# Performance work log

Hardware: AMD Instinct MI355X
Metric: run time of the kernel (lower is better)

## Reference

```python
import jax, jax.numpy as jnp
import numpy as np

N_NODES = 10000
N_EDGES = 100000
IN_FEATS = 64
OUT_FEATS = 64
N_EDGE_TYPES = 10


def setup_inputs() -> dict:
    key = jax.random.key(0)
    k_feat, k_src, k_dst, k_ord, k_emb = jax.random.split(key, 5)
    feat = jax.random.normal(k_feat, (N_NODES, IN_FEATS), dtype=jnp.float32)
    src = jax.random.randint(k_src, (N_EDGES,), 0, N_NODES, dtype=jnp.int32)
    dst = jax.random.randint(k_dst, (N_EDGES,), 0, N_NODES, dtype=jnp.int32)
    order = jax.random.randint(k_ord, (N_EDGES,), 0, N_EDGE_TYPES, dtype=jnp.int32)
    # xavier-uniform-like init for the relation-weight embedding table
    emb_weight = jax.random.normal(k_emb, (N_EDGE_TYPES, IN_FEATS * OUT_FEATS), dtype=jnp.float32) * 0.02
    bias = jnp.zeros((OUT_FEATS,), dtype=jnp.float32)
    return {"feat": feat, "src": src, "dst": dst, "order": order,
            "emb_weight": emb_weight, "bias": bias}


def reference(feat, src, dst, order, emb_weight, bias):
    n_nodes, in_feats = feat.shape
    out_feats = emb_weight.shape[1] // in_feats
    n_edges = src.shape[0]
    ones_e = jnp.ones((n_edges,), dtype=feat.dtype)

    # norm='both': scale source features by out_degree^{-1/2}
    out_deg = jnp.clip(jax.ops.segment_sum(ones_e, src, num_segments=n_nodes), 1.0)
    feat_n = feat * (out_deg ** -0.5)[:, None]

    # per-edge relation weight gather: [E, out, in]
    w = emb_weight[order].reshape(n_edges, out_feats, in_feats)
    h_src = feat_n[src]                              # [E, in]
    msg = jnp.einsum('eoi,ei->eo', w, h_src)         # [E, out]

    # scatter-sum aggregate to destination nodes
    rst = jax.ops.segment_sum(msg, dst, num_segments=n_nodes)  # [N, out]

    # post-norm by in_degree^{-1/2}
    in_deg = jnp.clip(jax.ops.segment_sum(ones_e, dst, num_segments=n_nodes), 1.0)
    rst = rst * (in_deg ** -0.5)[:, None]
    return rst + bias
```

## Files before the change

kernel.cpp:

```cpp
#include <hip/hip_runtime.h>
#include <stdint.h>


typedef __attribute__((ext_vector_type(8))) short short8;
typedef __attribute__((ext_vector_type(4))) float f32x4;

constexpr int N_NODES = 10000;
constexpr int N_EDGES = 100000;
constexpr int F = 64;
constexpr int R = 10;
constexpr int BLOCK = 256;
constexpr int EPG = 32;
constexpr int CAP = 16384;
constexpr int GPR = CAP / EPG;
constexpr int N_GROUPS = R * GPR;
constexpr int CAPN = 64;

union U8 { uint32_t u[4]; short8 s; };

__device__ inline uint32_t pk_hi(float x, float y) {
    uint32_t bx = __float_as_uint(x), by = __float_as_uint(y);
    return (bx >> 16) | (by & 0xFFFF0000u);
}
__device__ inline uint32_t pk_lo(float x, float y) {
    uint32_t bx = __float_as_uint(x), by = __float_as_uint(y);
    float lx = x - __uint_as_float(bx & 0xFFFF0000u);
    float ly = y - __uint_as_float(by & 0xFFFF0000u);
    return (__float_as_uint(lx) >> 16) | (__float_as_uint(ly) & 0xFFFF0000u);
}

__global__ void k_count(const int* __restrict__ src, const int* __restrict__ dst,
                        const int* __restrict__ order, const float* __restrict__ emb,
                        int* deg_out, int* deg_in, int* rel_cnt,
                        int* __restrict__ ssrc, uint4* __restrict__ wfrag,
                        int* __restrict__ dstbuf) {
    __shared__ int hist[R], base[R];
    int tid = threadIdx.x;
    int t = blockIdx.x * BLOCK + tid;
    if (tid < R) hist[tid] = 0;
    __syncthreads();
    int r = -1, lr = 0, s = 0, d = 0, rank = 0;
    if (t < N_EDGES) {
        s = src[t]; d = dst[t];
        atomicAdd(&deg_out[s], 1);
        rank = atomicAdd(&deg_in[d], 1);
        r = order[t];
        lr = atomicAdd(&hist[r], 1);
    }
    __syncthreads();
    if (tid < R) base[tid] = hist[tid] ? atomicAdd(&rel_cnt[tid], hist[tid]) : 0;
    __syncthreads();
    if (t < N_EDGES) {
        int slot = r * CAP + base[r] + lr;
        ssrc[slot] = s;
        if (rank < CAPN) dstbuf[d * CAPN + rank] = slot;
    }

    if (t < R * 16 * 64) {
        int lane = t & 63, frag = t >> 6;
        int p = frag & 1, ks = (frag >> 1) & 1, tt = (frag >> 2) & 3, rr = frag >> 4;
        int o = 16 * tt + (lane & 15), q = lane >> 4;
        const float* w = emb + (size_t)rr * F * F + (size_t)o * F + 32 * ks + 8 * q;
        float4 f0 = *(const float4*)w;
        float4 f1 = *(const float4*)(w + 4);
        uint4 v;
        if (p == 0) v = make_uint4(pk_hi(f0.x, f0.y), pk_hi(f0.z, f0.w),
                                   pk_hi(f1.x, f1.y), pk_hi(f1.z, f1.w));
        else        v = make_uint4(pk_lo(f0.x, f0.y), pk_lo(f0.z, f0.w),
                                   pk_lo(f1.x, f1.y), pk_lo(f1.z, f1.w));
        wfrag[(size_t)frag * 64 + lane] = v;
    }
}

__device__ inline void mk_afrag(const float* __restrict__ feat,
                                const int* __restrict__ deg_out,
                                int srow, int q,
                                U8& h0, U8& l0, U8& h1, U8& l1) {
    float nr = rsqrtf((float)max(deg_out[srow], 1));
    const float* row = feat + (size_t)srow * F + 8 * q;
    float4 f0 = *(const float4*)row;
    float4 f1 = *(const float4*)(row + 4);
    float4 f2 = *(const float4*)(row + 32);
    float4 f3 = *(const float4*)(row + 36);
    f0.x *= nr; f0.y *= nr; f0.z *= nr; f0.w *= nr;
    f1.x *= nr; f1.y *= nr; f1.z *= nr; f1.w *= nr;
    f2.x *= nr; f2.y *= nr; f2.z *= nr; f2.w *= nr;
    f3.x *= nr; f3.y *= nr; f3.z *= nr; f3.w *= nr;
    h0.u[0] = pk_hi(f0.x, f0.y); h0.u[1] = pk_hi(f0.z, f0.w);
    h0.u[2] = pk_hi(f1.x, f1.y); h0.u[3] = pk_hi(f1.z, f1.w);
    l0.u[0] = pk_lo(f0.x, f0.y); l0.u[1] = pk_lo(f0.z, f0.w);
    l0.u[2] = pk_lo(f1.x, f1.y); l0.u[3] = pk_lo(f1.z, f1.w);
    h1.u[0] = pk_hi(f2.x, f2.y); h1.u[1] = pk_hi(f2.z, f2.w);
    h1.u[2] = pk_hi(f3.x, f3.y); h1.u[3] = pk_hi(f3.z, f3.w);
    l1.u[0] = pk_lo(f2.x, f2.y); l1.u[1] = pk_lo(f2.z, f2.w);
    l1.u[2] = pk_lo(f3.x, f3.y); l1.u[3] = pk_lo(f3.z, f3.w);
}

__global__ __launch_bounds__(BLOCK, 3) void k_edge(
    const float* __restrict__ feat, const int* __restrict__ deg_out,
    const short8* __restrict__ wfrag, const int* __restrict__ rel_cnt,
    const int* __restrict__ ssrc, float* __restrict__ msg) {
    int lane = threadIdx.x & 63;
    int wib = threadIdx.x >> 6;
    int g = blockIdx.x * (BLOCK / 64) + wib;
    if (g >= N_GROUPS) return;
    int r = g >> 9;
    int e0 = (g & (GPR - 1)) * EPG;
    int cnt = rel_cnt[r];
    if (e0 >= cnt) return;

    int q = lane >> 4;
    int iA = e0 + (lane & 15), iB = iA + 16;
    const int* sr = ssrc + r * CAP;
    int sA = iA < cnt ? sr[iA] : 0;
    int sB = iB < cnt ? sr[iB] : 0;

    U8 Ah0, Al0, Ah1, Al1, Bh0, Bl0, Bh1, Bl1;
    mk_afrag(feat, deg_out, sA, q, Ah0, Al0, Ah1, Al1);
    mk_afrag(feat, deg_out, sB, q, Bh0, Bl0, Bh1, Bl1);

    const short8* wf = wfrag + (size_t)r * 16 * 64;
    f32x4 acc0[4], acc1[4];
#pragma unroll
    for (int t = 0; t < 4; ++t) {
        acc0[t] = (f32x4){0.f, 0.f, 0.f, 0.f};
        acc1[t] = (f32x4){0.f, 0.f, 0.f, 0.f};
    }

#pragma unroll
    for (int t = 0; t < 4; ++t) {
        short8 bh0 = wf[(t * 4 + 0) * 64 + lane];
        short8 bl0 = wf[(t * 4 + 1) * 64 + lane];
        short8 bh1 = wf[(t * 4 + 2) * 64 + lane];
        short8 bl1 = wf[(t * 4 + 3) * 64 + lane];
        f32x4 x = acc0[t], y = acc1[t];
        x = __builtin_amdgcn_mfma_f32_16x16x32_bf16(Al0.s, bh0, x, 0, 0, 0);
        y = __builtin_amdgcn_mfma_f32_16x16x32_bf16(Bl0.s, bh0, y, 0, 0, 0);
        x = __builtin_amdgcn_mfma_f32_16x16x32_bf16(Ah0.s, bl0, x, 0, 0, 0);
        y = __builtin_amdgcn_mfma_f32_16x16x32_bf16(Bh0.s, bl0, y, 0, 0, 0);
        x = __builtin_amdgcn_mfma_f32_16x16x32_bf16(Ah0.s, bh0, x, 0, 0, 0);
        y = __builtin_amdgcn_mfma_f32_16x16x32_bf16(Bh0.s, bh0, y, 0, 0, 0);
        x = __builtin_amdgcn_mfma_f32_16x16x32_bf16(Al1.s, bh1, x, 0, 0, 0);
        y = __builtin_amdgcn_mfma_f32_16x16x32_bf16(Bl1.s, bh1, y, 0, 0, 0);
        x = __builtin_amdgcn_mfma_f32_16x16x32_bf16(Ah1.s, bl1, x, 0, 0, 0);
        y = __builtin_amdgcn_mfma_f32_16x16x32_bf16(Bh1.s, bl1, y, 0, 0, 0);
        x = __builtin_amdgcn_mfma_f32_16x16x32_bf16(Ah1.s, bh1, x, 0, 0, 0);
        y = __builtin_amdgcn_mfma_f32_16x16x32_bf16(Bh1.s, bh1, y, 0, 0, 0);
        acc0[t] = x; acc1[t] = y;
    }

    float* mrow = msg + ((size_t)(r * CAP + e0)) * F;
    int col = lane & 15;
#pragma unroll
    for (int gg = 0; gg < 4; ++gg) {
        int row = q * 4 + gg;
#pragma unroll
        for (int t = 0; t < 4; ++t) {
            mrow[row * F + 16 * t + col] = acc0[t][gg];
            mrow[(row + 16) * F + 16 * t + col] = acc1[t][gg];
        }
    }
}

__global__ void k_agg(const float4* __restrict__ msg, const int* __restrict__ dstbuf,
                      const int* __restrict__ deg_in, const float* __restrict__ bias,
                      float4* __restrict__ out) {
    int t = blockIdx.x * BLOCK + threadIdx.x;
    if (t >= N_NODES * 16) return;
    int n = t >> 4, c4 = t & 15;
    int deg = deg_in[n];
    const int* dl = dstbuf + (size_t)n * CAPN;
    float4 acc = make_float4(0.f, 0.f, 0.f, 0.f);
    int k = 0;
    for (; k + 4 <= deg; k += 4) {
        int s0 = dl[k], s1 = dl[k + 1], s2 = dl[k + 2], s3 = dl[k + 3];
        float4 g0 = msg[(size_t)s0 * 16 + c4];
        float4 g1 = msg[(size_t)s1 * 16 + c4];
        float4 g2 = msg[(size_t)s2 * 16 + c4];
        float4 g3 = msg[(size_t)s3 * 16 + c4];
        acc.x += (g0.x + g1.x) + (g2.x + g3.x);
        acc.y += (g0.y + g1.y) + (g2.y + g3.y);
        acc.z += (g0.z + g1.z) + (g2.z + g3.z);
        acc.w += (g0.w + g1.w) + (g2.w + g3.w);
    }
    for (; k < deg; ++k) {
        float4 g = msg[(size_t)dl[k] * 16 + c4];
        acc.x += g.x; acc.y += g.y; acc.z += g.z; acc.w += g.w;
    }
    float sc = rsqrtf((float)max(deg, 1));
    float4 b = ((const float4*)bias)[c4];
    out[t] = make_float4(acc.x * sc + b.x, acc.y * sc + b.y,
                         acc.z * sc + b.z, acc.w * sc + b.w);
}

extern "C" void kernel_launch(void* const* d_in, const int* in_sizes, int n_in,
                              void* d_out, int out_size, void* d_ws, size_t ws_size,
                              hipStream_t stream) {
    const float* feat  = (const float*)d_in[0];
    const int*   src   = (const int*)d_in[1];
    const int*   dst   = (const int*)d_in[2];
    const int*   order = (const int*)d_in[3];
    const float* emb   = (const float*)d_in[4];
    const float* bias  = (const float*)d_in[5];
    float* out = (float*)d_out;

    int*   deg_out = (int*)d_ws;
    int*   deg_in  = deg_out + N_NODES;
    int*   rel_cnt = deg_in + N_NODES;
    int*   ssrc    = rel_cnt + 16;
    uint4* wfrag   = (uint4*)(ssrc + R * CAP);
    int*   dstbuf  = (int*)(wfrag + (size_t)R * 16 * 64);
    float* msg     = (float*)(dstbuf + (size_t)N_NODES * CAPN);

    size_t zbytes = (size_t)(2 * N_NODES + 16) * sizeof(int);
    hipMemsetAsync(d_ws, 0, zbytes, stream);

    int eb = (N_EDGES + BLOCK - 1) / BLOCK;
    k_count<<<eb, BLOCK, 0, stream>>>(src, dst, order, emb, deg_out, deg_in,
                                      rel_cnt, ssrc, wfrag, dstbuf);
    int gblocks = (N_GROUPS + (BLOCK / 64) - 1) / (BLOCK / 64);
    k_edge<<<gblocks, BLOCK, 0, stream>>>(feat, deg_out, (const short8*)wfrag,
                                          rel_cnt, ssrc, msg);
    int ab = (N_NODES * 16 + BLOCK - 1) / BLOCK;
    k_agg<<<ab, BLOCK, 0, stream>>>((const float4*)msg, dstbuf, deg_in, bias,
                                    (float4*)out);
}
```

Before: 104.8 us.

## Fold workspace zeroing into count kernel and compact edge-group grid

```diff
diff --git a/kernel.cpp b/kernel.cpp
--- a/kernel.cpp
+++ b/kernel.cpp
@@ -12,9 +12,12 @@
 constexpr int BLOCK = 256;
 constexpr int EPG = 32;
 constexpr int CAP = 16384;
-constexpr int GPR = CAP / EPG;
-constexpr int N_GROUPS = R * GPR;
 constexpr int CAPN = 64;
+constexpr int ZERO_INTS = 2 * N_NODES + 16;
+constexpr int ZB = (ZERO_INTS + BLOCK - 1) / BLOCK;
+constexpr int MAXG = N_EDGES / EPG + R;
+
+__device__ int g_zero_done;
 
 union U8 { uint32_t u[4]; short8 s; };
 
@@ -37,24 +40,23 @@
     __shared__ int hist[R], base[R];
     int tid = threadIdx.x;
     int t = blockIdx.x * BLOCK + tid;
+
+    bool active = t < N_EDGES;
+    int s = 0, d = 0, r = 0;
+    if (active) { s = src[t]; d = dst[t]; r = order[t]; }
     if (tid < R) hist[tid] = 0;
-    __syncthreads();
-    int r = -1, lr = 0, s = 0, d = 0, rank = 0;
-    if (t < N_EDGES) {
-        s = src[t]; d = dst[t];
-        atomicAdd(&deg_out[s], 1);
-        rank = atomicAdd(&deg_in[d], 1);
-        r = order[t];
-        lr = atomicAdd(&hist[r], 1);
-    }
-    __syncthreads();
-    if (tid < R) base[tid] = hist[tid] ? atomicAdd(&rel_cnt[tid], hist[tid]) : 0;
-    __syncthreads();
-    if (t < N_EDGES) {
-        int slot = r * CAP + base[r] + lr;
-        ssrc[slot] = s;
-        if (rank < CAPN) dstbuf[d * CAPN + rank] = slot;
-    }
+
+    if (blockIdx.x < ZB) {
+        if (t < ZERO_INTS) deg_out[t] = 0;
+        __threadfence();
+    }
+    __syncthreads();
+    if (blockIdx.x < ZB && tid == 0)
+        __hip_atomic_fetch_add(&g_zero_done, 1, __ATOMIC_RELEASE,
+                               __HIP_MEMORY_SCOPE_AGENT);
+
+    int lr = 0;
+    if (active) lr = atomicAdd(&hist[r], 1);
 
     if (t < R * 16 * 64) {
         int lane = t & 63, frag = t >> 6;
@@ -69,6 +71,27 @@
         else        v = make_uint4(pk_lo(f0.x, f0.y), pk_lo(f0.z, f0.w),
                                    pk_lo(f1.x, f1.y), pk_lo(f1.z, f1.w));
         wfrag[(size_t)frag * 64 + lane] = v;
+    }
+
+    if (tid == 0) {
+        while (__hip_atomic_load(&g_zero_done, __ATOMIC_ACQUIRE,
+                                 __HIP_MEMORY_SCOPE_AGENT) < ZB)
+            __builtin_amdgcn_s_sleep(1);
+    }
+    __syncthreads();
+
+    int rank = 0;
+    if (active) {
+        atomicAdd(&deg_out[s], 1);
+        rank = atomicAdd(&deg_in[d], 1);
+    }
+    __syncthreads();
+    if (tid < R) base[tid] = hist[tid] ? atomicAdd(&rel_cnt[tid], hist[tid]) : 0;
+    __syncthreads();
+    if (active) {
+        int slot = r * CAP + base[r] + lr;
+        ssrc[slot] = s;
+        if (rank < CAPN) dstbuf[d * CAPN + rank] = slot;
     }
 }
 
@@ -103,11 +126,17 @@
     int lane = threadIdx.x & 63;
     int wib = threadIdx.x >> 6;
     int g = blockIdx.x * (BLOCK / 64) + wib;
-    if (g >= N_GROUPS) return;
-    int r = g >> 9;
-    int e0 = (g & (GPR - 1)) * EPG;
-    int cnt = rel_cnt[r];
-    if (e0 >= cnt) return;
+
+    int r = -1, lg = 0, cnt = 0, cum = 0;
+#pragma unroll
+    for (int i = 0; i < R; ++i) {
+        int ci = rel_cnt[i];
+        int gi = (ci + EPG - 1) >> 5;
+        if (g >= cum && g < cum + gi) { r = i; lg = g - cum; cnt = ci; }
+        cum += gi;
+    }
+    if (r < 0) return;
+    int e0 = lg << 5;
 
     int q = lane >> 4;
     int iA = e0 + (lane & 15), iB = iA + 16;
@@ -166,6 +195,9 @@
                       const int* __restrict__ deg_in, const float* __restrict__ bias,
                       float4* __restrict__ out) {
     int t = blockIdx.x * BLOCK + threadIdx.x;
+    if (t == 0)
+        __hip_atomic_store(&g_zero_done, 0, __ATOMIC_RELAXED,
+                           __HIP_MEMORY_SCOPE_AGENT);
     if (t >= N_NODES * 16) return;
     int n = t >> 4, c4 = t & 15;
     int deg = deg_in[n];
@@ -212,13 +244,10 @@
     int*   dstbuf  = (int*)(wfrag + (size_t)R * 16 * 64);
     float* msg     = (float*)(dstbuf + (size_t)N_NODES * CAPN);
 
-    size_t zbytes = (size_t)(2 * N_NODES + 16) * sizeof(int);
-    hipMemsetAsync(d_ws, 0, zbytes, stream);
-
     int eb = (N_EDGES + BLOCK - 1) / BLOCK;
     k_count<<<eb, BLOCK, 0, stream>>>(src, dst, order, emb, deg_out, deg_in,
                                       rel_cnt, ssrc, wfrag, dstbuf);
-    int gblocks = (N_GROUPS + (BLOCK / 64) - 1) / (BLOCK / 64);
+    int gblocks = (MAXG + (BLOCK / 64) - 1) / (BLOCK / 64);
     k_edge<<<gblocks, BLOCK, 0, stream>>>(feat, deg_out, (const short8*)wfrag,
                                           rel_cnt, ssrc, msg);
     int ab = (N_NODES * 16 + BLOCK - 1) / BLOCK;
```

Measured after the change: 131.4 us. +25.4%, slower.

## Prepack node features to bf16 hi/lo once and compact edge-group grid

Applied to the files above, without the earlier changes.

```diff
diff --git a/kernel.cpp b/kernel.cpp
--- a/kernel.cpp
+++ b/kernel.cpp
@@ -12,9 +12,8 @@
 constexpr int BLOCK = 256;
 constexpr int EPG = 32;
 constexpr int CAP = 16384;
-constexpr int GPR = CAP / EPG;
-constexpr int N_GROUPS = R * GPR;
 constexpr int CAPN = 64;
+constexpr int MAXG = N_EDGES / EPG + R;
 
 union U8 { uint32_t u[4]; short8 s; };
 
@@ -31,9 +30,10 @@
 
 __global__ void k_count(const int* __restrict__ src, const int* __restrict__ dst,
                         const int* __restrict__ order, const float* __restrict__ emb,
+                        const float* __restrict__ feat,
                         int* deg_out, int* deg_in, int* rel_cnt,
                         int* __restrict__ ssrc, uint4* __restrict__ wfrag,
-                        int* __restrict__ dstbuf) {
+                        int* __restrict__ dstbuf, uint4* __restrict__ pfeat) {
     __shared__ int hist[R], base[R];
     int tid = threadIdx.x;
     int t = blockIdx.x * BLOCK + tid;
@@ -70,44 +70,44 @@
                                    pk_lo(f1.x, f1.y), pk_lo(f1.z, f1.w));
         wfrag[(size_t)frag * 64 + lane] = v;
     }
-}
-
-__device__ inline void mk_afrag(const float* __restrict__ feat,
-                                const int* __restrict__ deg_out,
-                                int srow, int q,
-                                U8& h0, U8& l0, U8& h1, U8& l1) {
-    float nr = rsqrtf((float)max(deg_out[srow], 1));
-    const float* row = feat + (size_t)srow * F + 8 * q;
-    float4 f0 = *(const float4*)row;
-    float4 f1 = *(const float4*)(row + 4);
-    float4 f2 = *(const float4*)(row + 32);
-    float4 f3 = *(const float4*)(row + 36);
-    f0.x *= nr; f0.y *= nr; f0.z *= nr; f0.w *= nr;
-    f1.x *= nr; f1.y *= nr; f1.z *= nr; f1.w *= nr;
-    f2.x *= nr; f2.y *= nr; f2.z *= nr; f2.w *= nr;
-    f3.x *= nr; f3.y *= nr; f3.z *= nr; f3.w *= nr;
-    h0.u[0] = pk_hi(f0.x, f0.y); h0.u[1] = pk_hi(f0.z, f0.w);
-    h0.u[2] = pk_hi(f1.x, f1.y); h0.u[3] = pk_hi(f1.z, f1.w);
-    l0.u[0] = pk_lo(f0.x, f0.y); l0.u[1] = pk_lo(f0.z, f0.w);
-    l0.u[2] = pk_lo(f1.x, f1.y); l0.u[3] = pk_lo(f1.z, f1.w);
-    h1.u[0] = pk_hi(f2.x, f2.y); h1.u[1] = pk_hi(f2.z, f2.w);
-    h1.u[2] = pk_hi(f3.x, f3.y); h1.u[3] = pk_hi(f3.z, f3.w);
-    l1.u[0] = pk_lo(f2.x, f2.y); l1.u[1] = pk_lo(f2.z, f2.w);
-    l1.u[2] = pk_lo(f3.x, f3.y); l1.u[3] = pk_lo(f3.z, f3.w);
+
+    if (t < N_NODES * 4) {
+        int n = t >> 2, p = t & 3;
+        const float* rp = feat + (size_t)n * F + 16 * p;
+        float4 a = *(const float4*)rp;
+        float4 b = *(const float4*)(rp + 4);
+        float4 c = *(const float4*)(rp + 8);
+        float4 e = *(const float4*)(rp + 12);
+        uint4* pf = pfeat + (size_t)n * 16;
+        pf[2 * p]     = make_uint4(pk_hi(a.x, a.y), pk_hi(a.z, a.w),
+                                   pk_hi(b.x, b.y), pk_hi(b.z, b.w));
+        pf[2 * p + 1] = make_uint4(pk_hi(c.x, c.y), pk_hi(c.z, c.w),
+                                   pk_hi(e.x, e.y), pk_hi(e.z, e.w));
+        pf[8 + 2 * p]     = make_uint4(pk_lo(a.x, a.y), pk_lo(a.z, a.w),
+                                       pk_lo(b.x, b.y), pk_lo(b.z, b.w));
+        pf[8 + 2 * p + 1] = make_uint4(pk_lo(c.x, c.y), pk_lo(c.z, c.w),
+                                       pk_lo(e.x, e.y), pk_lo(e.z, e.w));
+    }
 }
 
 __global__ __launch_bounds__(BLOCK, 3) void k_edge(
-    const float* __restrict__ feat, const int* __restrict__ deg_out,
+    const uint4* __restrict__ pfeat, const int* __restrict__ deg_out,
     const short8* __restrict__ wfrag, const int* __restrict__ rel_cnt,
     const int* __restrict__ ssrc, float* __restrict__ msg) {
     int lane = threadIdx.x & 63;
     int wib = threadIdx.x >> 6;
     int g = blockIdx.x * (BLOCK / 64) + wib;
-    if (g >= N_GROUPS) return;
-    int r = g >> 9;
-    int e0 = (g & (GPR - 1)) * EPG;
-    int cnt = rel_cnt[r];
-    if (e0 >= cnt) return;
+
+    int r = -1, lg = 0, cnt = 0, cum = 0;
+#pragma unroll
+    for (int i = 0; i < R; ++i) {
+        int ci = rel_cnt[i];
+        int gi = (ci + EPG - 1) >> 5;
+        if (g >= cum && g < cum + gi) { r = i; lg = g - cum; cnt = ci; }
+        cum += gi;
+    }
+    if (r < 0) return;
+    int e0 = lg << 5;
 
     int q = lane >> 4;
     int iA = e0 + (lane & 15), iB = iA + 16;
@@ -115,9 +115,13 @@
     int sA = iA < cnt ? sr[iA] : 0;
     int sB = iB < cnt ? sr[iB] : 0;
 
-    U8 Ah0, Al0, Ah1, Al1, Bh0, Bl0, Bh1, Bl1;
-    mk_afrag(feat, deg_out, sA, q, Ah0, Al0, Ah1, Al1);
-    mk_afrag(feat, deg_out, sB, q, Bh0, Bl0, Bh1, Bl1);
+    float nrA = rsqrtf((float)max(deg_out[sA], 1));
+    float nrB = rsqrtf((float)max(deg_out[sB], 1));
+
+    const short8* pA = (const short8*)(pfeat + (size_t)sA * 16);
+    const short8* pB = (const short8*)(pfeat + (size_t)sB * 16);
+    short8 Ah0 = pA[q], Ah1 = pA[4 + q], Al0 = pA[8 + q], Al1 = pA[12 + q];
+    short8 Bh0 = pB[q], Bh1 = pB[4 + q], Bl0 = pB[8 + q], Bl1 = pB[12 + q];
 
     const short8* wf = wfrag + (size_t)r * 16 * 64;
     f32x4 acc0[4], acc1[4];
@@ -134,18 +138,18 @@
         short8 bh1 = wf[(t * 4 + 2) * 64 + lane];
         short8 bl1 = wf[(t * 4 + 3) * 64 + lane];
         f32x4 x = acc0[t], y = acc1[t];
-        x = __builtin_amdgcn_mfma_f32_16x16x32_bf16(Al0.s, bh0, x, 0, 0, 0);
-        y = __builtin_amdgcn_mfma_f32_16x16x32_bf16(Bl0.s, bh0, y, 0, 0, 0);
-        x = __builtin_amdgcn_mfma_f32_16x16x32_bf16(Ah0.s, bl0, x, 0, 0, 0);
-        y = __builtin_amdgcn_mfma_f32_16x16x32_bf16(Bh0.s, bl0, y, 0, 0, 0);
-        x = __builtin_amdgcn_mfma_f32_16x16x32_bf16(Ah0.s, bh0, x, 0, 0, 0);
-        y = __builtin_amdgcn_mfma_f32_16x16x32_bf16(Bh0.s, bh0, y, 0, 0, 0);
-        x = __builtin_amdgcn_mfma_f32_16x16x32_bf16(Al1.s, bh1, x, 0, 0, 0);
-        y = __builtin_amdgcn_mfma_f32_16x16x32_bf16(Bl1.s, bh1, y, 0, 0, 0);
-        x = __builtin_amdgcn_mfma_f32_16x16x32_bf16(Ah1.s, bl1, x, 0, 0, 0);
-        y = __builtin_amdgcn_mfma_f32_16x16x32_bf16(Bh1.s, bl1, y, 0, 0, 0);
-        x = __builtin_amdgcn_mfma_f32_16x16x32_bf16(Ah1.s, bh1, x, 0, 0, 0);
-        y = __builtin_amdgcn_mfma_f32_16x16x32_bf16(Bh1.s, bh1, y, 0, 0, 0);
+        x = __builtin_amdgcn_mfma_f32_16x16x32_bf16(Al0, bh0, x, 0, 0, 0);
+        y = __builtin_amdgcn_mfma_f32_16x16x32_bf16(Bl0, bh0, y, 0, 0, 0);
+        x = __builtin_amdgcn_mfma_f32_16x16x32_bf16(Ah0, bl0, x, 0, 0, 0);
+        y = __builtin_amdgcn_mfma_f32_16x16x32_bf16(Bh0, bl0, y, 0, 0, 0);
+        x = __builtin_amdgcn_mfma_f32_16x16x32_bf16(Ah0, bh0, x, 0, 0, 0);
+        y = __builtin_amdgcn_mfma_f32_16x16x32_bf16(Bh0, bh0, y, 0, 0, 0);
+        x = __builtin_amdgcn_mfma_f32_16x16x32_bf16(Al1, bh1, x, 0, 0, 0);
+        y = __builtin_amdgcn_mfma_f32_16x16x32_bf16(Bl1, bh1, y, 0, 0, 0);
+        x = __builtin_amdgcn_mfma_f32_16x16x32_bf16(Ah1, bl1, x, 0, 0, 0);
+        y = __builtin_amdgcn_mfma_f32_16x16x32_bf16(Bh1, bl1, y, 0, 0, 0);
+        x = __builtin_amdgcn_mfma_f32_16x16x32_bf16(Ah1, bh1, x, 0, 0, 0);
+        y = __builtin_amdgcn_mfma_f32_16x16x32_bf16(Bh1, bh1, y, 0, 0, 0);
         acc0[t] = x; acc1[t] = y;
     }
 
@@ -154,10 +158,12 @@
 #pragma unroll
     for (int gg = 0; gg < 4; ++gg) {
         int row = q * 4 + gg;
+        float rA = __shfl(nrA, row);
+        float rB = __shfl(nrB, row);
 #pragma unroll
         for (int t = 0; t < 4; ++t) {
-            mrow[row * F + 16 * t + col] = acc0[t][gg];
-            mrow[(row + 16) * F + 16 * t + col] = acc1[t][gg];
+            mrow[row * F + 16 * t + col] = acc0[t][gg] * rA;
+            mrow[(row + 16) * F + 16 * t + col] = acc1[t][gg] * rB;
         }
     }
 }
@@ -210,16 +216,17 @@
     int*   ssrc    = rel_cnt + 16;
     uint4* wfrag   = (uint4*)(ssrc + R * CAP);
     int*   dstbuf  = (int*)(wfrag + (size_t)R * 16 * 64);
-    float* msg     = (float*)(dstbuf + (size_t)N_NODES * CAPN);
+    uint4* pfeat   = (uint4*)(dstbuf + (size_t)N_NODES * CAPN);
+    float* msg     = (float*)(pfeat + (size_t)N_NODES * 16);
 
     size_t zbytes = (size_t)(2 * N_NODES + 16) * sizeof(int);
     hipMemsetAsync(d_ws, 0, zbytes, stream);
 
     int eb = (N_EDGES + BLOCK - 1) / BLOCK;
-    k_count<<<eb, BLOCK, 0, stream>>>(src, dst, order, emb, deg_out, deg_in,
-                                      rel_cnt, ssrc, wfrag, dstbuf);
-    int gblocks = (N_GROUPS + (BLOCK / 64) - 1) / (BLOCK / 64);
-    k_edge<<<gblocks, BLOCK, 0, stream>>>(feat, deg_out, (const short8*)wfrag,
+    k_count<<<eb, BLOCK, 0, stream>>>(src, dst, order, emb, feat, deg_out, deg_in,
+                                      rel_cnt, ssrc, wfrag, dstbuf, pfeat);
+    int gblocks = (MAXG + (BLOCK / 64) - 1) / (BLOCK / 64);
+    k_edge<<<gblocks, BLOCK, 0, stream>>>(pfeat, deg_out, (const short8*)wfrag,
                                           rel_cnt, ssrc, msg);
     int ab = (N_NODES * 16 + BLOCK - 1) / BLOCK;
     k_agg<<<ab, BLOCK, 0, stream>>>((const float4*)msg, dstbuf, deg_in, bias,
```

Result: no change. 105.2 us (+0.4%).
